# Optimization experiments

Hardware: AMD Instinct MI355X
Metric: run time of the kernel (lower is better)

The kernel has to match this reference:

```python
import jax, jax.numpy as jnp
import numpy as np

B, L, E = 4, 2048, 1024
H, D = 16, 64  # heads, head_dim; H*D == E


def setup_inputs() -> dict:
    key = jax.random.key(0)
    ks = jax.random.split(key, 6)
    s = 0.02
    return {
        "x": jax.random.normal(ks[0], (B, L, E), dtype=jnp.float32),
        "Wq": jax.random.normal(ks[1], (E, H * D), dtype=jnp.float32) * s,
        "Wk": jax.random.normal(ks[2], (E, H * D), dtype=jnp.float32) * s,
        "Wv": jax.random.normal(ks[3], (E, H * D), dtype=jnp.float32) * s,
        "Wo": jax.random.normal(ks[4], (H * D, E), dtype=jnp.float32) * s,
        "bo": jax.random.normal(ks[5], (E,), dtype=jnp.float32) * s,
    }


def reference(x, Wq, Wk, Wv, Wo, bo):
    b, l, e = x.shape
    q = (x @ Wq).reshape(b, l, H, D)
    k = (x @ Wk).reshape(b, l, H, D)
    v = (x @ Wv).reshape(b, l, H, D)
    # NOTE: original scales by sqrt(embed_size), not sqrt(head_dim)
    energy = jnp.einsum('nqhd,nkhd->nhqk', q, k)
    attn = jax.nn.softmax(energy / jnp.sqrt(jnp.float32(e)), axis=3)
    out = jnp.einsum('nhql,nlhd->nqhd', attn, v).reshape(b, l, H * D)
    return out @ Wo + bo
```

## Files before the change

### kernel.cpp

```cpp
#include <hip/hip_runtime.h>

#define B_ 4
#define L_ 2048
#define E_ 1024
#define H_ 16
#define D_ 64
#define CSCALE 0.045084960222629414f

typedef short s16x8 __attribute__((ext_vector_type(8)));
typedef short s16x4 __attribute__((ext_vector_type(4)));
typedef float f32x4 __attribute__((ext_vector_type(4)));

__device__ __forceinline__ unsigned short f2bf(float f) {
  union { float f; unsigned int u; } v;
  v.f = f;
  unsigned int u = v.u;
  u += 0x7fffu + ((u >> 16) & 1u);
  return (unsigned short)(u >> 16);
}

__device__ __forceinline__ void async16(const void* g, void* l) {
  __builtin_amdgcn_global_load_lds(
      (__attribute__((address_space(1))) void*)(g),
      (__attribute__((address_space(3))) void*)(l), 16, 0, 0);
}

__device__ __forceinline__ s16x4 pack4bf(float p0, float p1, float p2, float p3) {
  union { float f; unsigned int u; } a0, a1, a2, a3;
  a0.f = p0; a1.f = p1; a2.f = p2; a3.f = p3;
  unsigned int r0 = a0.u + 0x8000u, r1 = a1.u + 0x8000u;
  unsigned int r2 = a2.u + 0x8000u, r3 = a3.u + 0x8000u;
  union { s16x4 v; unsigned int u[2]; } out;
  out.u[0] = __builtin_amdgcn_perm(r1, r0, 0x07060302);
  out.u[1] = __builtin_amdgcn_perm(r3, r2, 0x07060302);
  return out.v;
}

__global__ void k_prep(const float* __restrict__ x,
                       const float* __restrict__ Wq, const float* __restrict__ Wk,
                       const float* __restrict__ Wv, const float* __restrict__ Wo,
                       unsigned short* __restrict__ xb,
                       unsigned short* __restrict__ Wt, unsigned short* __restrict__ WoT) {
  __shared__ float t[32][33];
  int bid = blockIdx.x, tid = threadIdx.x;
  if (bid < 8192) {
    int i = bid * 256 + tid;
    float4 v = ((const float4*)x)[i];
    ushort4 o;
    o.x = f2bf(v.x); o.y = f2bf(v.y); o.z = f2bf(v.z); o.w = f2bf(v.w);
    ((ushort4*)xb)[i] = o;
    return;
  }
  int tt = bid - 8192;
  int wsel = tt >> 10, tile = tt & 1023;
  const float* in = (wsel == 0) ? Wq : (wsel == 1) ? Wk : (wsel == 2) ? Wv : Wo;
  unsigned short* out = (wsel == 0) ? Wt : (wsel == 1) ? Wt + (1u << 20)
                        : (wsel == 2) ? Wt + (2u << 20) : WoT;
  int bx = tile & 31, by = tile >> 5;
  int tx = tid & 31, ty = tid >> 5;
  int xcol = bx * 32 + tx;
  int y0 = by * 32;
#pragma unroll
  for (int i = 0; i < 4; ++i)
    t[ty + i * 8][tx] = in[(size_t)(y0 + ty + i * 8) * 1024 + xcol];
  __syncthreads();
  int xo = by * 32 + tx;
  int yo0 = bx * 32;
#pragma unroll
  for (int i = 0; i < 4; ++i)
    out[(size_t)(yo0 + ty + i * 8) * 1024 + xo] = f2bf(t[tx][ty + i * 8]);
}

__global__ __launch_bounds__(256) void k_gemm_qkvt(
    const unsigned short* __restrict__ xb, const unsigned short* __restrict__ Wt,
    unsigned short* __restrict__ Qb, unsigned short* __restrict__ Kb,
    unsigned short* __restrict__ Vt) {
  __shared__ __align__(16) unsigned short As[128 * 32];
  __shared__ __align__(16) unsigned short Bs[128 * 32];
  const int bid = blockIdx.x;
  const int tid = threadIdx.x;
  const int w = tid >> 6, lane = tid & 63;
  const int quad = lane >> 4, mrow = lane & 15;
  const bool isQK = bid < 1024;
  int m0, n0;
  const unsigned short *PA, *PB;
  if (isQK) {
    m0 = (bid & 63) * 128;
    n0 = (bid >> 6) * 128;
    PA = xb + (size_t)m0 * 1024;
    PB = Wt + (size_t)n0 * 1024;
  } else {
    int g = bid - 1024;
    m0 = (g & 7) * 128;
    n0 = (g >> 3) * 128;
    PA = Wt + (2u << 20) + (size_t)m0 * 1024;
    PB = xb + (size_t)n0 * 1024;
  }
  const int wr = (w >> 1) * 64, wc = (w & 1) * 64;
  const f32x4 fz = {0.f, 0.f, 0.f, 0.f};
  f32x4 acc[4][4];
#pragma unroll
  for (int a = 0; a < 4; ++a)
#pragma unroll
    for (int b = 0; b < 4; ++b) acc[a][b] = fz;

  for (int kt = 0; kt < 32; ++kt) {
    __syncthreads();
#pragma unroll
    for (int r = 0; r < 2; ++r) {
      int c = r * 256 + tid;
      int row = c >> 2, cc = c & 3;
      async16(PA + (size_t)row * 1024 + kt * 32 + cc * 8, &As[c * 8]);
    }
#pragma unroll
    for (int r = 0; r < 2; ++r) {
      int c = r * 256 + tid;
      int row = c >> 2, cc = c & 3;
      async16(PB + (size_t)row * 1024 + kt * 32 + cc * 8, &Bs[c * 8]);
    }
    __syncthreads();
    s16x8 a[4], b[4];
#pragma unroll
    for (int mt = 0; mt < 4; ++mt)
      a[mt] = *(const s16x8*)&As[(wr + mt * 16 + mrow) * 32 + quad * 8];
#pragma unroll
    for (int nt = 0; nt < 4; ++nt)
      b[nt] = *(const s16x8*)&Bs[(wc + nt * 16 + mrow) * 32 + quad * 8];
#pragma unroll
    for (int mt = 0; mt < 4; ++mt)
#pragma unroll
      for (int nt = 0; nt < 4; ++nt)
        acc[mt][nt] = __builtin_amdgcn_mfma_f32_16x16x32_bf16(a[mt], b[nt], acc[mt][nt], 0, 0, 0);
  }
  if (isQK) {
#pragma unroll
    for (int mt = 0; mt < 4; ++mt)
#pragma unroll
      for (int nt = 0; nt < 4; ++nt)
#pragma unroll
        for (int i = 0; i < 4; ++i) {
          int row = m0 + wr + mt * 16 + quad * 4 + i;
          int col = n0 + wc + nt * 16 + mrow;
          int bb = row >> 11, l = row & 2047;
          if (col < 1024) {
            int h = col >> 6, d = col & 63;
            Qb[(((size_t)(bb * 16 + h)) * 2048 + l) * 64 + d] = f2bf(acc[mt][nt][i]);
          } else {
            int c2 = col - 1024, h = c2 >> 6, d = c2 & 63;
            Kb[(((size_t)(bb * 16 + h)) * 2048 + l) * 64 + d] = f2bf(acc[mt][nt][i] * CSCALE);
          }
        }
  } else {
#pragma unroll
    for (int mt = 0; mt < 4; ++mt)
#pragma unroll
      for (int nt = 0; nt < 4; ++nt)
#pragma unroll
        for (int i = 0; i < 4; ++i) {
          int f = m0 + wr + mt * 16 + quad * 4 + i;
          int tk = n0 + wc + nt * 16 + mrow;
          int bb = tk >> 11, l = tk & 2047;
          Vt[((size_t)(bb * 1024 + f)) * 2048 + l] = f2bf(acc[mt][nt][i]);
        }
  }
}

__global__ __launch_bounds__(256, 2) void k_attn(
    const unsigned short* __restrict__ Qb, const unsigned short* __restrict__ Kb,
    const unsigned short* __restrict__ Vt, unsigned short* __restrict__ AO) {
  __shared__ __align__(16) unsigned short KVs[2][8192];
  const int tid = threadIdx.x, w = tid >> 6, lane = tid & 63;
  const int quad = lane >> 4, mrow = lane & 15;
  const int bh = blockIdx.x & 63;
  const int q0 = (blockIdx.x >> 6) * 128;
  const unsigned short* Qh = Qb + (size_t)bh * 2048 * 64;
  const unsigned short* Kh = Kb + (size_t)bh * 2048 * 64;
  const unsigned short* Vh = Vt + (size_t)bh * 64 * 2048;
  unsigned short* KVf = &KVs[0][0];

#pragma unroll
  for (int r = 0; r < 4; ++r) {
    int c = r * 256 + tid;
    int row = c >> 3, cl = c & 7;
    int gc = cl ^ (row & 7);
    async16(Qh + (size_t)(q0 + row) * 64 + gc * 8, &KVf[c * 8]);
  }
  __syncthreads();
  s16x8 qb[2][2];
#pragma unroll
  for (int nt = 0; nt < 2; ++nt)
#pragma unroll
    for (int ks = 0; ks < 2; ++ks) {
      int row = w * 32 + nt * 16 + mrow;
      qb[nt][ks] = *(const s16x8*)&KVf[row * 64 + (((ks * 4 + quad) ^ (row & 7)) << 3)];
    }
  __syncthreads();

#pragma unroll
  for (int r = 0; r < 2; ++r) {
    int c = r * 256 + tid;
    int row = c >> 3, cl = c & 7;
    int gc = cl ^ (row & 7);
    async16(Kh + (size_t)row * 64 + gc * 8, &KVs[0][c * 8]);
  }
#pragma unroll
  for (int r = 0; r < 2; ++r) {
    int c = r * 256 + tid;
    int row = c >> 3, cl = c & 7;
    int gc = cl ^ (row & 7);
    async16(Vh + (size_t)row * 2048 + gc * 8, &KVs[0][4096 + c * 8]);
  }

  const f32x4 fz = {0.f, 0.f, 0.f, 0.f};
  f32x4 o[2][4];
  float lr[2];
#pragma unroll
  for (int nt = 0; nt < 2; ++nt) {
    lr[nt] = 0.f;
#pragma unroll
    for (int dt = 0; dt < 4; ++dt) o[nt][dt] = fz;
  }
  s16x4 vbp[4][4];
  s16x4 pap[4][2];

  for (int j = 0; j < 32; ++j) {
    __syncthreads();
    const unsigned short* Kt = &KVs[j & 1][0];
    const unsigned short* Vs = &KVs[j & 1][4096];

    s16x8 ak[4][2];
#pragma unroll
    for (int mt = 0; mt < 4; ++mt)
#pragma unroll
      for (int ks = 0; ks < 2; ++ks) {
        int row = mt * 16 + mrow;
        ak[mt][ks] = *(const s16x8*)&Kt[row * 64 + (((ks * 4 + quad) ^ (row & 7)) << 3)];
      }
    s16x4 vb[4][4];
#pragma unroll
    for (int dt = 0; dt < 4; ++dt)
#pragma unroll
      for (int lt = 0; lt < 4; ++lt) {
        int row = dt * 16 + mrow;
        int lbase = lt * 16 + quad * 4;
        int cg = lbase >> 3, off = lbase & 7;
        vb[dt][lt] = *(const s16x4*)&Vs[row * 64 + ((cg ^ (row & 7)) << 3) + off];
      }

    if (j + 1 < 32) {
      unsigned short* nb = &KVs[(j + 1) & 1][0];
#pragma unroll
      for (int r = 0; r < 2; ++r) {
        int c = r * 256 + tid;
        int row = c >> 3, cl = c & 7;
        int gc = cl ^ (row & 7);
        async16(Kh + (size_t)((j + 1) * 64 + row) * 64 + gc * 8, &nb[c * 8]);
      }
#pragma unroll
      for (int r = 0; r < 2; ++r) {
        int c = r * 256 + tid;
        int row = c >> 3, cl = c & 7;
        int gc = cl ^ (row & 7);
        async16(Vh + (size_t)row * 2048 + (j + 1) * 64 + gc * 8, &nb[4096 + c * 8]);
      }
    }

    f32x4 s[4][2];
#pragma unroll
    for (int mt = 0; mt < 4; ++mt)
#pragma unroll
      for (int nt = 0; nt < 2; ++nt) s[mt][nt] = fz;
#pragma unroll
    for (int ks = 0; ks < 2; ++ks)
#pragma unroll
      for (int mt = 0; mt < 4; ++mt)
#pragma unroll
        for (int nt = 0; nt < 2; ++nt)
          s[mt][nt] = __builtin_amdgcn_mfma_f32_16x16x32_bf16(ak[mt][ks], qb[nt][ks], s[mt][nt], 0, 0, 0);

    if (j) {
#pragma unroll
      for (int nt = 0; nt < 2; ++nt)
#pragma unroll
        for (int dt = 0; dt < 4; ++dt)
#pragma unroll
          for (int lt = 0; lt < 4; ++lt)
            o[nt][dt] = __builtin_amdgcn_mfma_f32_16x16x16bf16_1k(pap[lt][nt], vbp[dt][lt], o[nt][dt], 0, 0, 0);
    }

#pragma unroll
    for (int mt = 0; mt < 4; ++mt)
#pragma unroll
      for (int nt = 0; nt < 2; ++nt) {
        float p0 = __builtin_amdgcn_exp2f(s[mt][nt][0]);
        float p1 = __builtin_amdgcn_exp2f(s[mt][nt][1]);
        float p2 = __builtin_amdgcn_exp2f(s[mt][nt][2]);
        float p3 = __builtin_amdgcn_exp2f(s[mt][nt][3]);
        lr[nt] += (p0 + p1) + (p2 + p3);
        pap[mt][nt] = pack4bf(p0, p1, p2, p3);
      }
#pragma unroll
    for (int dt = 0; dt < 4; ++dt)
#pragma unroll
      for (int lt = 0; lt < 4; ++lt) vbp[dt][lt] = vb[dt][lt];
  }
#pragma unroll
  for (int nt = 0; nt < 2; ++nt)
#pragma unroll
    for (int dt = 0; dt < 4; ++dt)
#pragma unroll
      for (int lt = 0; lt < 4; ++lt)
        o[nt][dt] = __builtin_amdgcn_mfma_f32_16x16x16bf16_1k(pap[lt][nt], vbp[dt][lt], o[nt][dt], 0, 0, 0);

#pragma unroll
  for (int nt = 0; nt < 2; ++nt) {
    float v = lr[nt];
    v += __shfl_xor(v, 16);
    v += __shfl_xor(v, 32);
    lr[nt] = v;
  }

  int b_ = bh >> 4, h = bh & 15;
#pragma unroll
  for (int nt = 0; nt < 2; ++nt)
#pragma unroll
    for (int i = 0; i < 4; ++i) {
      float inv = 1.f / __shfl(lr[nt], quad * 4 + i, 64);
      int qrow = q0 + w * 32 + nt * 16 + quad * 4 + i;
#pragma unroll
      for (int dt = 0; dt < 4; ++dt) {
        int d = dt * 16 + mrow;
        AO[((size_t)(b_ * 2048 + qrow)) * 1024 + h * 64 + d] = f2bf(o[nt][dt][i] * inv);
      }
    }
}

__global__ __launch_bounds__(256) void k_gemm_out(
    const unsigned short* __restrict__ Ab, const unsigned short* __restrict__ WoT,
    const float* __restrict__ bo, float* __restrict__ out) {
  __shared__ __align__(16) unsigned short As[128 * 32];
  __shared__ __align__(16) unsigned short Bs[128 * 32];
  const int tid = threadIdx.x;
  const int w = tid >> 6, lane = tid & 63;
  const int quad = lane >> 4, mrow = lane & 15;
  const int m0 = blockIdx.x * 128, n0 = blockIdx.y * 128;
  const int wr = (w >> 1) * 64, wc = (w & 1) * 64;
  const f32x4 fz = {0.f, 0.f, 0.f, 0.f};
  f32x4 acc[4][4];
#pragma unroll
  for (int a = 0; a < 4; ++a)
#pragma unroll
    for (int b = 0; b < 4; ++b) acc[a][b] = fz;

  for (int kt = 0; kt < 32; ++kt) {
    __syncthreads();
#pragma unroll
    for (int r = 0; r < 2; ++r) {
      int c = r * 256 + tid;
      int row = c >> 2, cc = c & 3;
      async16(Ab + (size_t)(m0 + row) * 1024 + kt * 32 + cc * 8, &As[c * 8]);
    }
#pragma unroll
    for (int r = 0; r < 2; ++r) {
      int c = r * 256 + tid;
      int row = c >> 2, cc = c & 3;
      async16(WoT + (size_t)(n0 + row) * 1024 + kt * 32 + cc * 8, &Bs[c * 8]);
    }
    __syncthreads();
    s16x8 a[4], b[4];
#pragma unroll
    for (int mt = 0; mt < 4; ++mt)
      a[mt] = *(const s16x8*)&As[(wr + mt * 16 + mrow) * 32 + quad * 8];
#pragma unroll
    for (int nt = 0; nt < 4; ++nt)
      b[nt] = *(const s16x8*)&Bs[(wc + nt * 16 + mrow) * 32 + quad * 8];
#pragma unroll
    for (int mt = 0; mt < 4; ++mt)
#pragma unroll
      for (int nt = 0; nt < 4; ++nt)
        acc[mt][nt] = __builtin_amdgcn_mfma_f32_16x16x32_bf16(a[mt], b[nt], acc[mt][nt], 0, 0, 0);
  }
#pragma unroll
  for (int mt = 0; mt < 4; ++mt)
#pragma unroll
    for (int nt = 0; nt < 4; ++nt)
#pragma unroll
      for (int i = 0; i < 4; ++i) {
        int row = m0 + wr + mt * 16 + quad * 4 + i;
        int col = n0 + wc + nt * 16 + mrow;
        out[(size_t)row * 1024 + col] = acc[mt][nt][i] + bo[col];
      }
}

extern "C" void kernel_launch(void* const* d_in, const int* in_sizes, int n_in,
                              void* d_out, int out_size, void* d_ws, size_t ws_size,
                              hipStream_t stream) {
  const float* x  = (const float*)d_in[0];
  const float* Wq = (const float*)d_in[1];
  const float* Wk = (const float*)d_in[2];
  const float* Wv = (const float*)d_in[3];
  const float* Wo = (const float*)d_in[4];
  const float* bo = (const float*)d_in[5];
  float* out = (float*)d_out;

  char* ws = (char*)d_ws;
  const size_t MiB = 1u << 20;
  unsigned short* xb  = (unsigned short*)(ws);
  unsigned short* Wt  = (unsigned short*)(ws + 16 * MiB);
  unsigned short* WoT = (unsigned short*)(ws + 22 * MiB);
  unsigned short* Qb  = (unsigned short*)(ws + 24 * MiB);
  unsigned short* Kb  = (unsigned short*)(ws + 40 * MiB);
  unsigned short* Vt  = (unsigned short*)(ws + 56 * MiB);
  unsigned short* AO  = xb;

  k_prep<<<12288, 256, 0, stream>>>(x, Wq, Wk, Wv, Wo, xb, Wt, WoT);
  k_gemm_qkvt<<<1536, 256, 0, stream>>>(xb, Wt, Qb, Kb, Vt);
  k_attn<<<1024, 256, 0, stream>>>(Qb, Kb, Vt, AO);
  k_gemm_out<<<dim3(64, 8), 256, 0, stream>>>(AO, WoT, bo, out);
}
```

Baseline: 286.4 us.

## Triple-buffer K/V tiles in attention with partial vmcnt waits and higher occupancy

Changes the attention kernel's K/V staging from double to triple buffering in shared memory. Two tiles are prefetched up front, and each iteration waits only for the oldest outstanding loads using explicit s_waitcnt immediates before a raw barrier. The previous software pipeline that carried P and V across iterations is removed in favour of a straight-line compute per tile. Launch bounds are raised to 4 blocks per CU, which limits registers per thread and may cause spills. The extra buffer adds shared memory per block, and the hard-coded waitcnt encodings must match the number of loads in flight.

```diff
diff --git a/kernel.cpp b/kernel.cpp
--- a/kernel.cpp
+++ b/kernel.cpp
@@ -165,10 +165,10 @@
   }
 }
 
-__global__ __launch_bounds__(256, 2) void k_attn(
+__global__ __launch_bounds__(256, 4) void k_attn(
     const unsigned short* __restrict__ Qb, const unsigned short* __restrict__ Kb,
     const unsigned short* __restrict__ Vt, unsigned short* __restrict__ AO) {
-  __shared__ __align__(16) unsigned short KVs[2][8192];
+  __shared__ __align__(16) unsigned short KVs[3][8192];
   const int tid = threadIdx.x, w = tid >> 6, lane = tid & 63;
   const int quad = lane >> 4, mrow = lane & 15;
   const int bh = blockIdx.x & 63;
@@ -176,14 +176,30 @@
   const unsigned short* Qh = Qb + (size_t)bh * 2048 * 64;
   const unsigned short* Kh = Kb + (size_t)bh * 2048 * 64;
   const unsigned short* Vh = Vt + (size_t)bh * 64 * 2048;
-  unsigned short* KVf = &KVs[0][0];
 
 #pragma unroll
   for (int r = 0; r < 4; ++r) {
     int c = r * 256 + tid;
     int row = c >> 3, cl = c & 7;
     int gc = cl ^ (row & 7);
-    async16(Qh + (size_t)(q0 + row) * 64 + gc * 8, &KVf[c * 8]);
+    async16(Qh + (size_t)(q0 + row) * 64 + gc * 8, &KVs[2][c * 8]);
+  }
+#pragma unroll
+  for (int j0 = 0; j0 < 2; ++j0) {
+#pragma unroll
+    for (int r = 0; r < 2; ++r) {
+      int c = r * 256 + tid;
+      int row = c >> 3, cl = c & 7;
+      int gc = cl ^ (row & 7);
+      async16(Kh + (size_t)(j0 * 64 + row) * 64 + gc * 8, &KVs[j0][c * 8]);
+    }
+#pragma unroll
+    for (int r = 0; r < 2; ++r) {
+      int c = r * 256 + tid;
+      int row = c >> 3, cl = c & 7;
+      int gc = cl ^ (row & 7);
+      async16(Vh + (size_t)row * 2048 + j0 * 64 + gc * 8, &KVs[j0][4096 + c * 8]);
+    }
   }
   __syncthreads();
   s16x8 qb[2][2];
@@ -192,24 +208,9 @@
 #pragma unroll
     for (int ks = 0; ks < 2; ++ks) {
       int row = w * 32 + nt * 16 + mrow;
-      qb[nt][ks] = *(const s16x8*)&KVf[row * 64 + (((ks * 4 + quad) ^ (row & 7)) << 3)];
+      qb[nt][ks] = *(const s16x8*)&KVs[2][row * 64 + (((ks * 4 + quad) ^ (row & 7)) << 3)];
     }
   __syncthreads();
-
-#pragma unroll
-  for (int r = 0; r < 2; ++r) {
-    int c = r * 256 + tid;
-    int row = c >> 3, cl = c & 7;
-    int gc = cl ^ (row & 7);
-    async16(Kh + (size_t)row * 64 + gc * 8, &KVs[0][c * 8]);
-  }
-#pragma unroll
-  for (int r = 0; r < 2; ++r) {
-    int c = r * 256 + tid;
-    int row = c >> 3, cl = c & 7;
-    int gc = cl ^ (row & 7);
-    async16(Vh + (size_t)row * 2048 + gc * 8, &KVs[0][4096 + c * 8]);
-  }
 
   const f32x4 fz = {0.f, 0.f, 0.f, 0.f};
   f32x4 o[2][4];
@@ -220,97 +221,89 @@
 #pragma unroll
     for (int dt = 0; dt < 4; ++dt) o[nt][dt] = fz;
   }
-  s16x4 vbp[4][4];
-  s16x4 pap[4][2];
-
-  for (int j = 0; j < 32; ++j) {
-    __syncthreads();
-    const unsigned short* Kt = &KVs[j & 1][0];
-    const unsigned short* Vs = &KVs[j & 1][4096];
-
-    s16x8 ak[4][2];
-#pragma unroll
-    for (int mt = 0; mt < 4; ++mt)
-#pragma unroll
-      for (int ks = 0; ks < 2; ++ks) {
-        int row = mt * 16 + mrow;
-        ak[mt][ks] = *(const s16x8*)&Kt[row * 64 + (((ks * 4 + quad) ^ (row & 7)) << 3)];
-      }
-    s16x4 vb[4][4];
-#pragma unroll
-    for (int dt = 0; dt < 4; ++dt)
-#pragma unroll
-      for (int lt = 0; lt < 4; ++lt) {
-        int row = dt * 16 + mrow;
-        int lbase = lt * 16 + quad * 4;
-        int cg = lbase >> 3, off = lbase & 7;
-        vb[dt][lt] = *(const s16x4*)&Vs[row * 64 + ((cg ^ (row & 7)) << 3) + off];
-      }
-
-    if (j + 1 < 32) {
-      unsigned short* nb = &KVs[(j + 1) & 1][0];
-#pragma unroll
-      for (int r = 0; r < 2; ++r) {
-        int c = r * 256 + tid;
-        int row = c >> 3, cl = c & 7;
-        int gc = cl ^ (row & 7);
-        async16(Kh + (size_t)((j + 1) * 64 + row) * 64 + gc * 8, &nb[c * 8]);
-      }
-#pragma unroll
-      for (int r = 0; r < 2; ++r) {
-        int c = r * 256 + tid;
-        int row = c >> 3, cl = c & 7;
-        int gc = cl ^ (row & 7);
-        async16(Vh + (size_t)row * 2048 + (j + 1) * 64 + gc * 8, &nb[4096 + c * 8]);
-      }
-    }
-
-    f32x4 s[4][2];
-#pragma unroll
-    for (int mt = 0; mt < 4; ++mt)
-#pragma unroll
-      for (int nt = 0; nt < 2; ++nt) s[mt][nt] = fz;
-#pragma unroll
-    for (int ks = 0; ks < 2; ++ks)
-#pragma unroll
-      for (int mt = 0; mt < 4; ++mt)
-#pragma unroll
-        for (int nt = 0; nt < 2; ++nt)
-          s[mt][nt] = __builtin_amdgcn_mfma_f32_16x16x32_bf16(ak[mt][ks], qb[nt][ks], s[mt][nt], 0, 0, 0);
-
-    if (j) {
-#pragma unroll
-      for (int nt = 0; nt < 2; ++nt)
-#pragma unroll
-        for (int dt = 0; dt < 4; ++dt)
-#pragma unroll
-          for (int lt = 0; lt < 4; ++lt)
-            o[nt][dt] = __builtin_amdgcn_mfma_f32_16x16x16bf16_1k(pap[lt][nt], vbp[dt][lt], o[nt][dt], 0, 0, 0);
-    }
-
-#pragma unroll
-    for (int mt = 0; mt < 4; ++mt)
-#pragma unroll
-      for (int nt = 0; nt < 2; ++nt) {
-        float p0 = __builtin_amdgcn_exp2f(s[mt][nt][0]);
-        float p1 = __builtin_amdgcn_exp2f(s[mt][nt][1]);
-        float p2 = __builtin_amdgcn_exp2f(s[mt][nt][2]);
-        float p3 = __builtin_amdgcn_exp2f(s[mt][nt][3]);
-        lr[nt] += (p0 + p1) + (p2 + p3);
-        pap[mt][nt] = pack4bf(p0, p1, p2, p3);
-      }
-#pragma unroll
-    for (int dt = 0; dt < 4; ++dt)
-#pragma unroll
-      for (int lt = 0; lt < 4; ++lt) vbp[dt][lt] = vb[dt][lt];
-  }
-#pragma unroll
-  for (int nt = 0; nt < 2; ++nt)
-#pragma unroll
-    for (int dt = 0; dt < 4; ++dt)
-#pragma unroll
-      for (int lt = 0; lt < 4; ++lt)
-        o[nt][dt] = __builtin_amdgcn_mfma_f32_16x16x16bf16_1k(pap[lt][nt], vbp[dt][lt], o[nt][dt], 0, 0, 0);
+
+#define ATTN_BODY(J, SLOT, NSLOT, WAITIMM, PF)                                   \
+  {                                                                              \
+    __builtin_amdgcn_s_waitcnt(WAITIMM);                                         \
+    __builtin_amdgcn_s_barrier();                                                \
+    const unsigned short* Kt = &KVs[SLOT][0];                                    \
+    const unsigned short* Vs = &KVs[SLOT][4096];                                 \
+    s16x8 ak[4][2];                                                              \
+    _Pragma("unroll")                                                            \
+    for (int mt = 0; mt < 4; ++mt)                                               \
+      _Pragma("unroll")                                                          \
+      for (int ks = 0; ks < 2; ++ks) {                                           \
+        int row = mt * 16 + mrow;                                                \
+        ak[mt][ks] = *(const s16x8*)&Kt[row * 64 + (((ks * 4 + quad) ^ (row & 7)) << 3)]; \
+      }                                                                          \
+    s16x4 vb[4][4];                                                              \
+    _Pragma("unroll")                                                            \
+    for (int dt = 0; dt < 4; ++dt)                                               \
+      _Pragma("unroll")                                                          \
+      for (int lt = 0; lt < 4; ++lt) {                                           \
+        int row = dt * 16 + mrow;                                                \
+        int lbase = lt * 16 + quad * 4;                                          \
+        int cg = lbase >> 3, off = lbase & 7;                                    \
+        vb[dt][lt] = *(const s16x4*)&Vs[row * 64 + ((cg ^ (row & 7)) << 3) + off]; \
+      }                                                                          \
+    if (PF) {                                                                    \
+      unsigned short* nb = &KVs[NSLOT][0];                                       \
+      _Pragma("unroll")                                                          \
+      for (int r = 0; r < 2; ++r) {                                              \
+        int c = r * 256 + tid;                                                   \
+        int row = c >> 3, cl = c & 7;                                            \
+        int gc = cl ^ (row & 7);                                                 \
+        async16(Kh + (size_t)(((J) + 2) * 64 + row) * 64 + gc * 8, &nb[c * 8]);  \
+      }                                                                          \
+      _Pragma("unroll")                                                          \
+      for (int r = 0; r < 2; ++r) {                                              \
+        int c = r * 256 + tid;                                                   \
+        int row = c >> 3, cl = c & 7;                                            \
+        int gc = cl ^ (row & 7);                                                 \
+        async16(Vh + (size_t)row * 2048 + ((J) + 2) * 64 + gc * 8, &nb[4096 + c * 8]); \
+      }                                                                          \
+    }                                                                            \
+    f32x4 s[4][2];                                                               \
+    _Pragma("unroll")                                                            \
+    for (int mt = 0; mt < 4; ++mt)                                               \
+      _Pragma("unroll")                                                          \
+      for (int nt = 0; nt < 2; ++nt) s[mt][nt] = fz;                             \
+    _Pragma("unroll")                                                            \
+    for (int ks = 0; ks < 2; ++ks)                                               \
+      _Pragma("unroll")                                                          \
+      for (int mt = 0; mt < 4; ++mt)                                             \
+        _Pragma("unroll")                                                        \
+        for (int nt = 0; nt < 2; ++nt)                                           \
+          s[mt][nt] = __builtin_amdgcn_mfma_f32_16x16x32_bf16(ak[mt][ks], qb[nt][ks], s[mt][nt], 0, 0, 0); \
+    s16x4 pa[4][2];                                                              \
+    _Pragma("unroll")                                                            \
+    for (int mt = 0; mt < 4; ++mt)                                               \
+      _Pragma("unroll")                                                          \
+      for (int nt = 0; nt < 2; ++nt) {                                           \
+        float p0 = __builtin_amdgcn_exp2f(s[mt][nt][0]);                         \
+        float p1 = __builtin_amdgcn_exp2f(s[mt][nt][1]);                         \
+        float p2 = __builtin_amdgcn_exp2f(s[mt][nt][2]);                         \
+        float p3 = __builtin_amdgcn_exp2f(s[mt][nt][3]);                         \
+        lr[nt] += (p0 + p1) + (p2 + p3);                                         \
+        pa[mt][nt] = pack4bf(p0, p1, p2, p3);                                    \
+      }                                                                          \
+    _Pragma("unroll")                                                            \
+    for (int nt = 0; nt < 2; ++nt)                                               \
+      _Pragma("unroll")                                                          \
+      for (int dt = 0; dt < 4; ++dt)                                             \
+        _Pragma("unroll")                                                        \
+        for (int lt = 0; lt < 4; ++lt)                                           \
+          o[nt][dt] = __builtin_amdgcn_mfma_f32_16x16x16bf16_1k(pa[lt][nt], vb[dt][lt], o[nt][dt], 0, 0, 0); \
+  }
+
+  for (int jb = 0; jb < 30; jb += 3) {
+    ATTN_BODY(jb, 0, 2, 0xF74, 1);
+    ATTN_BODY(jb + 1, 1, 0, 0xF74, 1);
+    ATTN_BODY(jb + 2, 2, 1, 0xF74, 1);
+  }
+  ATTN_BODY(30, 0, 2, 0xF74, 0);
+  ATTN_BODY(31, 1, 0, 0xF70, 0);
+#undef ATTN_BODY
 
 #pragma unroll
   for (int nt = 0; nt < 2; ++nt) {
```

After: 288.8 us. Within noise of the previous version (+0.8%).
